# Optimization experiments

Hardware: AMD Instinct MI355X
Metric: run time of the kernel (lower is better)

The kernel has to match this reference:

```python
import jax, jax.numpy as jnp
import numpy as np


def setup_inputs() -> dict:
    key = jax.random.key(0)
    k1, k2, k3, k4 = jax.random.split(key, 4)
    B, D, C, N = 8192, 2048, 2048, 8
    x = jax.random.normal(k1, (B, D), dtype=jnp.float32)
    W = jax.random.normal(k2, (N, C, D), dtype=jnp.float32) * (1.0 / np.sqrt(D))
    b = jax.random.normal(k3, (N, C), dtype=jnp.float32) * 0.02
    factor = jnp.full((N,), 1.0 / N, dtype=jnp.float32)
    return {"x": x, "W": W, "b": b, "factor": factor}


def reference(x, W, b, factor):
    # Per-head linear: heads[b, n, c] = x @ W[n].T + b[n]
    heads = jnp.einsum("bd,ncd->bnc", x, W) + b[None, :, :]
    # Weighted sum over heads with canonical_factor (torch: cat(...,-1) @ factor)
    out = jnp.einsum("bnc,n->bc", heads, factor)
    return out
```

## Files before the change

kernel.cpp:

```cpp
#include <hip/hip_runtime.h>


#define MDIM 8192
#define KDIM 2048
#define NDIM 2048
#define NHEADS 8

#define BM 128
#define BN 128
#define BK 64

using bf16x8 = __attribute__((ext_vector_type(8))) short;
using f32x4  = __attribute__((ext_vector_type(4))) float;

__device__ __forceinline__ unsigned short f2bf(float x) {
    unsigned int u = __float_as_uint(x);
    u += 0x7FFFu + ((u >> 16) & 1u);
    return (unsigned short)(u >> 16);
}

__device__ __forceinline__ void async_load16(const void* g, void* l) {
    __builtin_amdgcn_global_load_lds(
        (const __attribute__((address_space(1))) unsigned int*)g,
        (__attribute__((address_space(3))) unsigned int*)l,
        16, 0, 0);
}

__global__ void reduce_W_kernel(const float* __restrict__ W,
                                const float* __restrict__ factor,
                                unsigned short* __restrict__ Wbf) {
    const size_t CD = (size_t)NDIM * KDIM;
    size_t idx = ((size_t)blockIdx.x * blockDim.x + threadIdx.x) * 4;
    float f[NHEADS];
#pragma unroll
    for (int n = 0; n < NHEADS; ++n) f[n] = factor[n];
    float ax = 0.f, ay = 0.f, az = 0.f, aw = 0.f;
#pragma unroll
    for (int n = 0; n < NHEADS; ++n) {
        float4 v = *reinterpret_cast<const float4*>(W + (size_t)n * CD + idx);
        ax += f[n] * v.x; ay += f[n] * v.y; az += f[n] * v.z; aw += f[n] * v.w;
    }
    ushort4 o;
    o.x = f2bf(ax); o.y = f2bf(ay); o.z = f2bf(az); o.w = f2bf(aw);
    *reinterpret_cast<ushort4*>(Wbf + idx) = o;
}

__global__ void cast_x_kernel(const float* __restrict__ x,
                              unsigned short* __restrict__ xbf) {
    size_t idx = ((size_t)blockIdx.x * blockDim.x + threadIdx.x) * 4;
    float4 v = *reinterpret_cast<const float4*>(x + idx);
    ushort4 o;
    o.x = f2bf(v.x); o.y = f2bf(v.y); o.z = f2bf(v.z); o.w = f2bf(v.w);
    *reinterpret_cast<ushort4*>(xbf + idx) = o;
}

__global__ void bias_kernel(const float* __restrict__ b,
                            const float* __restrict__ factor,
                            float* __restrict__ beff) {
    int c = blockIdx.x * blockDim.x + threadIdx.x;
    if (c < NDIM) {
        float s = 0.f;
#pragma unroll
        for (int n = 0; n < NHEADS; ++n) s += factor[n] * b[(size_t)n * NDIM + c];
        beff[c] = s;
    }
}

__global__ __launch_bounds__(256) void gemm_bt_kernel(
    const unsigned short* __restrict__ A,
    const unsigned short* __restrict__ B,
    const float* __restrict__ bias,
    float* __restrict__ C)
{
    __shared__ unsigned short As[BM * BK];
    __shared__ unsigned short Bs[BN * BK];

    const int tid  = threadIdx.x;
    const int lane = tid & 63;
    const int w    = tid >> 6;
    const int m16  = lane & 15;
    const int quad = lane >> 4;

    const int blockN0 = blockIdx.x * BN;
    const int blockM0 = blockIdx.y * BM;

    const int wr = (w >> 1) * 64;
    const int wc = (w & 1) * 64;

    const int srow = lane >> 3;
    const int scol = (lane & 7) * 8;
    const unsigned short* aP[4];
    const unsigned short* bP[4];
    unsigned short* aL[4];
    unsigned short* bL[4];
#pragma unroll
    for (int i = 0; i < 4; ++i) {
        int r = i * 32 + w * 8;
        aP[i] = A + (size_t)(blockM0 + r + srow) * KDIM + scol;
        bP[i] = B + (size_t)(blockN0 + r + srow) * KDIM + scol;
        aL[i] = As + (size_t)r * BK;
        bL[i] = Bs + (size_t)r * BK;
    }

    f32x4 acc[4][4] = {};

    for (int k0 = 0; k0 < KDIM; k0 += BK) {
#pragma unroll
        for (int i = 0; i < 4; ++i) {
            async_load16(aP[i], aL[i]);
            async_load16(bP[i], bL[i]);
            aP[i] += BK; bP[i] += BK;
        }
        __syncthreads();

#pragma unroll
        for (int kk = 0; kk < BK; kk += 32) {
            bf16x8 af[4], bfr[4];
#pragma unroll
            for (int rt = 0; rt < 4; ++rt)
                af[rt] = *reinterpret_cast<const bf16x8*>(
                    &As[(size_t)(wr + rt * 16 + m16) * BK + kk + quad * 8]);
#pragma unroll
            for (int ct = 0; ct < 4; ++ct)
                bfr[ct] = *reinterpret_cast<const bf16x8*>(
                    &Bs[(size_t)(wc + ct * 16 + m16) * BK + kk + quad * 8]);
#pragma unroll
            for (int rt = 0; rt < 4; ++rt)
#pragma unroll
                for (int ct = 0; ct < 4; ++ct)
                    acc[rt][ct] = __builtin_amdgcn_mfma_f32_16x16x32_bf16(
                        af[rt], bfr[ct], acc[rt][ct], 0, 0, 0);
        }
        __syncthreads();
    }

    float bv[4];
#pragma unroll
    for (int ct = 0; ct < 4; ++ct) bv[ct] = bias[blockN0 + wc + ct * 16 + m16];
#pragma unroll
    for (int rt = 0; rt < 4; ++rt) {
        int row0 = blockM0 + wr + rt * 16 + quad * 4;
#pragma unroll
        for (int ct = 0; ct < 4; ++ct) {
            int col = blockN0 + wc + ct * 16 + m16;
#pragma unroll
            for (int r = 0; r < 4; ++r)
                C[(size_t)(row0 + r) * NDIM + col] = acc[rt][ct][r] + bv[ct];
        }
    }
}

extern "C" void kernel_launch(void* const* d_in, const int* in_sizes, int n_in,
                              void* d_out, int out_size, void* d_ws, size_t ws_size,
                              hipStream_t stream) {
    const float* x      = (const float*)d_in[0];
    const float* W      = (const float*)d_in[1];
    const float* b      = (const float*)d_in[2];
    const float* factor = (const float*)d_in[3];
    float* out = (float*)d_out;

    unsigned short* xbf = (unsigned short*)d_ws;
    unsigned short* Wbf = (unsigned short*)((char*)d_ws + 33554432);
    float*          beff = (float*)((char*)d_ws + 33554432 + 8388608);

    reduce_W_kernel<<<dim3((NDIM * KDIM / 4) / 256), dim3(256), 0, stream>>>(W, factor, Wbf);
    cast_x_kernel<<<dim3(((size_t)MDIM * KDIM / 4) / 256), dim3(256), 0, stream>>>(x, xbf);
    bias_kernel<<<dim3(NDIM / 256), dim3(256), 0, stream>>>(b, factor, beff);

    gemm_bt_kernel<<<dim3(NDIM / BN, MDIM / BM), dim3(256), 0, stream>>>(xbf, Wbf, beff, out);
}
```

Before: 355.3 us.

## Fuse prep kernels, swizzle LDS layout, and remap GEMM block order

```diff
diff --git a/kernel.cpp b/kernel.cpp
--- a/kernel.cpp
+++ b/kernel.cpp
@@ -26,39 +26,37 @@
         16, 0, 0);
 }
 
-__global__ void reduce_W_kernel(const float* __restrict__ W,
-                                const float* __restrict__ factor,
-                                unsigned short* __restrict__ Wbf) {
-    const size_t CD = (size_t)NDIM * KDIM;
-    size_t idx = ((size_t)blockIdx.x * blockDim.x + threadIdx.x) * 4;
-    float f[NHEADS];
+__global__ void prep_kernel(const float* __restrict__ x,
+                            const float* __restrict__ W,
+                            const float* __restrict__ b,
+                            const float* __restrict__ factor,
+                            unsigned short* __restrict__ xbf,
+                            unsigned short* __restrict__ Wbf,
+                            float* __restrict__ beff) {
+    const int blk = blockIdx.x;
+    if (blk < 4096) {
+        const size_t CD = (size_t)NDIM * KDIM;
+        size_t idx = ((size_t)blk * blockDim.x + threadIdx.x) * 4;
+        float f[NHEADS];
 #pragma unroll
-    for (int n = 0; n < NHEADS; ++n) f[n] = factor[n];
-    float ax = 0.f, ay = 0.f, az = 0.f, aw = 0.f;
+        for (int n = 0; n < NHEADS; ++n) f[n] = factor[n];
+        float ax = 0.f, ay = 0.f, az = 0.f, aw = 0.f;
 #pragma unroll
-    for (int n = 0; n < NHEADS; ++n) {
-        float4 v = *reinterpret_cast<const float4*>(W + (size_t)n * CD + idx);
-        ax += f[n] * v.x; ay += f[n] * v.y; az += f[n] * v.z; aw += f[n] * v.w;
-    }
-    ushort4 o;
-    o.x = f2bf(ax); o.y = f2bf(ay); o.z = f2bf(az); o.w = f2bf(aw);
-    *reinterpret_cast<ushort4*>(Wbf + idx) = o;
-}
-
-__global__ void cast_x_kernel(const float* __restrict__ x,
-                              unsigned short* __restrict__ xbf) {
-    size_t idx = ((size_t)blockIdx.x * blockDim.x + threadIdx.x) * 4;
-    float4 v = *reinterpret_cast<const float4*>(x + idx);
-    ushort4 o;
-    o.x = f2bf(v.x); o.y = f2bf(v.y); o.z = f2bf(v.z); o.w = f2bf(v.w);
-    *reinterpret_cast<ushort4*>(xbf + idx) = o;
-}
-
-__global__ void bias_kernel(const float* __restrict__ b,
-                            const float* __restrict__ factor,
-                            float* __restrict__ beff) {
-    int c = blockIdx.x * blockDim.x + threadIdx.x;
-    if (c < NDIM) {
+        for (int n = 0; n < NHEADS; ++n) {
+            float4 v = *reinterpret_cast<const float4*>(W + (size_t)n * CD + idx);
+            ax += f[n] * v.x; ay += f[n] * v.y; az += f[n] * v.z; aw += f[n] * v.w;
+        }
+        ushort4 o;
+        o.x = f2bf(ax); o.y = f2bf(ay); o.z = f2bf(az); o.w = f2bf(aw);
+        *reinterpret_cast<ushort4*>(Wbf + idx) = o;
+    } else if (blk < 20480) {
+        size_t idx = ((size_t)(blk - 4096) * blockDim.x + threadIdx.x) * 4;
+        float4 v = *reinterpret_cast<const float4*>(x + idx);
+        ushort4 o;
+        o.x = f2bf(v.x); o.y = f2bf(v.y); o.z = f2bf(v.z); o.w = f2bf(v.w);
+        *reinterpret_cast<ushort4*>(xbf + idx) = o;
+    } else {
+        int c = (blk - 20480) * blockDim.x + threadIdx.x;
         float s = 0.f;
 #pragma unroll
         for (int n = 0; n < NHEADS; ++n) s += factor[n] * b[(size_t)n * NDIM + c];
@@ -81,14 +79,18 @@
     const int m16  = lane & 15;
     const int quad = lane >> 4;
 
-    const int blockN0 = blockIdx.x * BN;
-    const int blockM0 = blockIdx.y * BM;
+    const int bid = blockIdx.x;
+    const int g   = bid >> 3;
+    const int nt  = (bid & 7) * 2 + (g & 1);
+    const int mt  = g >> 1;
+    const int blockN0 = nt * BN;
+    const int blockM0 = mt * BM;
 
     const int wr = (w >> 1) * 64;
     const int wc = (w & 1) * 64;
 
     const int srow = lane >> 3;
-    const int scol = (lane & 7) * 8;
+    const int scol = ((lane & 7) ^ srow) * 8;
     const unsigned short* aP[4];
     const unsigned short* bP[4];
     unsigned short* aL[4];
@@ -117,13 +119,17 @@
         for (int kk = 0; kk < BK; kk += 32) {
             bf16x8 af[4], bfr[4];
 #pragma unroll
-            for (int rt = 0; rt < 4; ++rt)
-                af[rt] = *reinterpret_cast<const bf16x8*>(
-                    &As[(size_t)(wr + rt * 16 + m16) * BK + kk + quad * 8]);
+            for (int rt = 0; rt < 4; ++rt) {
+                int row = wr + rt * 16 + m16;
+                int gA = ((kk >> 3) + quad) ^ (row & 7);
+                af[rt] = *reinterpret_cast<const bf16x8*>(&As[(size_t)row * BK + gA * 8]);
+            }
 #pragma unroll
-            for (int ct = 0; ct < 4; ++ct)
-                bfr[ct] = *reinterpret_cast<const bf16x8*>(
-                    &Bs[(size_t)(wc + ct * 16 + m16) * BK + kk + quad * 8]);
+            for (int ct = 0; ct < 4; ++ct) {
+                int row = wc + ct * 16 + m16;
+                int gB = ((kk >> 3) + quad) ^ (row & 7);
+                bfr[ct] = *reinterpret_cast<const bf16x8*>(&Bs[(size_t)row * BK + gB * 8]);
+            }
 #pragma unroll
             for (int rt = 0; rt < 4; ++rt)
 #pragma unroll
@@ -159,13 +165,10 @@
     const float* factor = (const float*)d_in[3];
     float* out = (float*)d_out;
 
-    unsigned short* xbf = (unsigned short*)d_ws;
-    unsigned short* Wbf = (unsigned short*)((char*)d_ws + 33554432);
+    unsigned short* xbf  = (unsigned short*)d_ws;
+    unsigned short* Wbf  = (unsigned short*)((char*)d_ws + 33554432);
     float*          beff = (float*)((char*)d_ws + 33554432 + 8388608);
 
-    reduce_W_kernel<<<dim3((NDIM * KDIM / 4) / 256), dim3(256), 0, stream>>>(W, factor, Wbf);
-    cast_x_kernel<<<dim3(((size_t)MDIM * KDIM / 4) / 256), dim3(256), 0, stream>>>(x, xbf);
-    bias_kernel<<<dim3(NDIM / 256), dim3(256), 0, stream>>>(b, factor, beff);
-
-    gemm_bt_kernel<<<dim3(NDIM / BN, MDIM / BM), dim3(256), 0, stream>>>(xbf, Wbf, beff, out);
+    prep_kernel<<<dim3(20488), dim3(256), 0, stream>>>(x, W, b, factor, xbf, Wbf, beff);
+    gemm_bt_kernel<<<dim3(1024), dim3(256), 0, stream>>>(xbf, Wbf, beff, out);
 }
```

New measurement: 328.8 us. 7.5% less time.
